# Kernel tuning notes

Measured on AMD Instinct MI355X. Metric: run time of the kernel, lower is better.

The kernel has to match this reference:

```python
import jax, jax.numpy as jnp
import numpy as np

N = 500_000      # total nodes across all graphs in batch
B = 128          # batch_size (number of graphs)
S = 128          # state_size
D = 128          # aggregated_size


def setup_inputs() -> dict:
    key = jax.random.key(0)
    k1, k2, k3, k4, k5, k6 = jax.random.split(key, 6)
    nodes = jax.random.normal(k1, (N, S), dtype=jnp.float32)
    owner_masks = jax.random.randint(k2, (B, N), 0, 2, dtype=jnp.int32)
    # Linear params (torch Linear: y = x @ W.T + b); store W as [in, out] for x @ W
    scale = 1.0 / np.sqrt(S)
    Wt = jax.random.uniform(k3, (S, D), jnp.float32, -scale, scale)
    bt = jax.random.uniform(k4, (D,), jnp.float32, -scale, scale)
    Wg = jax.random.uniform(k5, (S, D), jnp.float32, -scale, scale)
    bg = jax.random.uniform(k6, (D,), jnp.float32, -scale, scale)
    return {"nodes": nodes, "owner_masks": owner_masks,
            "Wt": Wt, "bt": bt, "Wg": Wg, "bg": bg}


def reference(nodes, owner_masks, Wt, bt, Wg, bg):
    # gates = sigmoid(nodes @ Wg + bg)   [N, D]
    gates = jax.nn.sigmoid(nodes @ Wg + bg)
    # data = nodes @ Wt + bt             [N, D]
    data = nodes @ Wt + bt
    # pooled = owner_masks.float() @ (data * gates)   [B, D]
    return owner_masks.astype(jnp.float32) @ (data * gates)
```

## Files before the change

kernel.cpp:

```cpp
#include <hip/hip_runtime.h>


#define NTOT   500000
#define NBLK   512
#define NCHUNK 15625

typedef __attribute__((ext_vector_type(8))) unsigned short ushort8;
typedef __bf16 bf16x8 __attribute__((ext_vector_type(8)));
typedef __attribute__((ext_vector_type(4))) float f32x4;

static __device__ __forceinline__ unsigned short f2bf(float f) {
  unsigned int u = __float_as_uint(f);
  u += 0x7fffu + ((u >> 16) & 1u);
  return (unsigned short)(u >> 16);
}

static __device__ __forceinline__ unsigned long long pack4(unsigned short a, unsigned short b,
                                                           unsigned short c, unsigned short d) {
  return (unsigned long long)a | ((unsigned long long)b << 16) |
         ((unsigned long long)c << 32) | ((unsigned long long)d << 48);
}

template <bool ATOMIC>
__global__ __launch_bounds__(256, 2)
void agg_main(const float* __restrict__ nodes, const int* __restrict__ masks,
              const float* __restrict__ Wt, const float* __restrict__ bt,
              const float* __restrict__ Wg, const float* __restrict__ bg,
              float* __restrict__ outp) {
  __shared__ __align__(16) unsigned short nodes_s[32][136];
  __shared__ __align__(16) unsigned short mask_s[128][40];
  __shared__ __align__(16) unsigned short vt_s[128][40];

  const int tid = threadIdx.x;
  const int lane = tid & 63;
  const int w = tid >> 6;
  const int q = lane >> 4;
  const int r = lane & 15;

  bf16x8 Wf[2][4][2];
  float btr[2], bgr[2];
#pragma unroll
  for (int nt = 0; nt < 2; ++nt) {
    const int d = w * 32 + nt * 16 + r;
    btr[nt] = bt[d];
    bgr[nt] = bg[d];
#pragma unroll
    for (int ks = 0; ks < 4; ++ks) {
      ushort8 ft, fg;
#pragma unroll
      for (int j = 0; j < 8; ++j) {
        const int k = ks * 32 + q * 8 + j;
        ft[j] = f2bf(Wt[k * 128 + d]);
        fg[j] = f2bf(Wg[k * 128 + d]);
      }
      Wf[0][ks][nt] = __builtin_bit_cast(bf16x8, ft);
      Wf[1][ks][nt] = __builtin_bit_cast(bf16x8, fg);
    }
  }

  f32x4 acc[4][4];
  const f32x4 fzero = {0.f, 0.f, 0.f, 0.f};
#pragma unroll
  for (int i = 0; i < 4; ++i)
#pragma unroll
    for (int j = 0; j < 4; ++j) acc[i][j] = fzero;

  const int bid = blockIdx.x;
  const int c0 = (int)(((long long)bid * NCHUNK) / NBLK);
  const int c1 = (int)(((long long)(bid + 1) * NCHUNK) / NBLK);

  float4 nf[4];
  int4 mi[4];
  auto issue = [&](int c) {
    const int k0 = c * 32;
#pragma unroll
    for (int it = 0; it < 4; ++it) {
      const int flat = it * 256 + tid;
      const int nrow = flat >> 5, nc4 = flat & 31;
      nf[it] = *(const float4*)(nodes + (size_t)(k0 + nrow) * 128 + nc4 * 4);
      const int mrow = flat >> 3, mc4 = flat & 7;
      mi[it] = *(const int4*)(masks + (size_t)mrow * NTOT + k0 + mc4 * 4);
    }
  };

  if (c0 < c1) issue(c0);

  for (int c = c0; c < c1; ++c) {
    __syncthreads();
#pragma unroll
    for (int it = 0; it < 4; ++it) {
      const int flat = it * 256 + tid;
      const int nrow = flat >> 5, nc4 = flat & 31;
      *(unsigned long long*)&nodes_s[nrow][nc4 * 4] =
          pack4(f2bf(nf[it].x), f2bf(nf[it].y), f2bf(nf[it].z), f2bf(nf[it].w));
      const int mrow = flat >> 3, mc4 = flat & 7;
      *(unsigned long long*)&mask_s[mrow][mc4 * 4] =
          pack4(f2bf((float)mi[it].x), f2bf((float)mi[it].y),
                f2bf((float)mi[it].z), f2bf((float)mi[it].w));
    }
    __syncthreads();
    if (c + 1 < c1) issue(c + 1);

    f32x4 aD[2][2], aG[2][2];
#pragma unroll
    for (int i = 0; i < 2; ++i)
#pragma unroll
      for (int j = 0; j < 2; ++j) { aD[i][j] = fzero; aG[i][j] = fzero; }
#pragma unroll
    for (int ks = 0; ks < 4; ++ks) {
      bf16x8 a0 = *(const bf16x8*)&nodes_s[r][ks * 32 + q * 8];
      bf16x8 a1 = *(const bf16x8*)&nodes_s[16 + r][ks * 32 + q * 8];
#pragma unroll
      for (int nt = 0; nt < 2; ++nt) {
        aD[0][nt] = __builtin_amdgcn_mfma_f32_16x16x32_bf16(a0, Wf[0][ks][nt], aD[0][nt], 0, 0, 0);
        aD[1][nt] = __builtin_amdgcn_mfma_f32_16x16x32_bf16(a1, Wf[0][ks][nt], aD[1][nt], 0, 0, 0);
        aG[0][nt] = __builtin_amdgcn_mfma_f32_16x16x32_bf16(a0, Wf[1][ks][nt], aG[0][nt], 0, 0, 0);
        aG[1][nt] = __builtin_amdgcn_mfma_f32_16x16x32_bf16(a1, Wf[1][ks][nt], aG[1][nt], 0, 0, 0);
      }
    }

#pragma unroll
    for (int mt = 0; mt < 2; ++mt)
#pragma unroll
      for (int nt = 0; nt < 2; ++nt) {
        const int d = w * 32 + nt * 16 + r;
        unsigned short t[4];
#pragma unroll
        for (int reg = 0; reg < 4; ++reg) {
          const float x = aD[mt][nt][reg] + btr[nt];
          const float g = aG[mt][nt][reg] + bgr[nt];
          t[reg] = f2bf(x / (1.f + __expf(-g)));
        }
        *(unsigned long long*)&vt_s[d][mt * 16 + q * 4] = pack4(t[0], t[1], t[2], t[3]);
      }
    __syncthreads();

    const int mb = (w >> 1) * 64, nb = (w & 1) * 64;
    bf16x8 bfr[4];
#pragma unroll
    for (int nt = 0; nt < 4; ++nt)
      bfr[nt] = *(const bf16x8*)&vt_s[nb + nt * 16 + r][q * 8];
#pragma unroll
    for (int mt = 0; mt < 4; ++mt) {
      bf16x8 af = *(const bf16x8*)&mask_s[mb + mt * 16 + r][q * 8];
#pragma unroll
      for (int nt = 0; nt < 4; ++nt)
        acc[mt][nt] = __builtin_amdgcn_mfma_f32_16x16x32_bf16(af, bfr[nt], acc[mt][nt], 0, 0, 0);
    }
  }

#pragma unroll
  for (int mt = 0; mt < 4; ++mt)
#pragma unroll
    for (int nt = 0; nt < 4; ++nt)
#pragma unroll
      for (int reg = 0; reg < 4; ++reg) {
        const int b = (w >> 1) * 64 + mt * 16 + q * 4 + reg;
        const int d = (w & 1) * 64 + nt * 16 + r;
        if (ATOMIC)
          atomicAdd(&outp[b * 128 + d], acc[mt][nt][reg]);
        else
          outp[(size_t)bid * 16384 + b * 128 + d] = acc[mt][nt][reg];
      }
}

__global__ __launch_bounds__(256)
void agg_reduce(const float* __restrict__ part, float* __restrict__ out) {
  const int gid = blockIdx.x * 256 + threadIdx.x;
  const int i = gid & 16383;
  const int grp = gid >> 14;
  const float* p = part + (size_t)grp * 64 * 16384 + i;
  float s = 0.f;
#pragma unroll 8
  for (int g = 0; g < 64; ++g) s += p[(size_t)g * 16384];
  atomicAdd(&out[i], s);
}

extern "C" void kernel_launch(void* const* d_in, const int* in_sizes, int n_in,
                              void* d_out, int out_size, void* d_ws, size_t ws_size,
                              hipStream_t stream) {
  const float* nodes = (const float*)d_in[0];
  const int*   masks = (const int*)d_in[1];
  const float* Wt    = (const float*)d_in[2];
  const float* bt    = (const float*)d_in[3];
  const float* Wg    = (const float*)d_in[4];
  const float* bg    = (const float*)d_in[5];
  float* out = (float*)d_out;

  hipMemsetAsync(d_out, 0, (size_t)out_size * sizeof(float), stream);

  const size_t need = (size_t)NBLK * 16384 * sizeof(float);
  if (ws_size >= need) {
    agg_main<false><<<NBLK, 256, 0, stream>>>(nodes, masks, Wt, bt, Wg, bg, (float*)d_ws);
    agg_reduce<<<512, 256, 0, stream>>>((const float*)d_ws, out);
  } else {
    agg_main<true><<<NBLK, 256, 0, stream>>>(nodes, masks, Wt, bt, Wg, bg, out);
  }
}
```

Baseline: 523.8 us.

## Feed mask fragments from registers and double-buffer LDS with one barrier per chunk

Masks are now loaded straight into MFMA A-operand registers and turned into bf16 0/1 by bit selection, so the mask LDS tile and its staging pass are gone. The node and value tiles are double-buffered, and the pooling MFMA for chunk i-1 overlaps the projection GEMM for chunk i, cutting barriers from three per chunk to one. The manual float-to-bf16 routine is replaced by native bf16 conversion, and the sigmoid division by a reciprocal. Per-lane mask loads now cover shorter contiguous runs, so global access is less coalesced, and the pipelined register state raises register pressure.

```diff
diff --git a/kernel.cpp b/kernel.cpp
--- a/kernel.cpp
+++ b/kernel.cpp
@@ -7,18 +7,18 @@
 
 typedef __attribute__((ext_vector_type(8))) unsigned short ushort8;
 typedef __bf16 bf16x8 __attribute__((ext_vector_type(8)));
+typedef __bf16 bf16x2 __attribute__((ext_vector_type(2)));
 typedef __attribute__((ext_vector_type(4))) float f32x4;
 
-static __device__ __forceinline__ unsigned short f2bf(float f) {
-  unsigned int u = __float_as_uint(f);
-  u += 0x7fffu + ((u >> 16) & 1u);
-  return (unsigned short)(u >> 16);
-}
-
-static __device__ __forceinline__ unsigned long long pack4(unsigned short a, unsigned short b,
-                                                           unsigned short c, unsigned short d) {
-  return (unsigned long long)a | ((unsigned long long)b << 16) |
-         ((unsigned long long)c << 32) | ((unsigned long long)d << 48);
+static __device__ __forceinline__ unsigned int pkbf(float a, float b) {
+  bf16x2 v;
+  v[0] = (__bf16)a;
+  v[1] = (__bf16)b;
+  return __builtin_bit_cast(unsigned int, v);
+}
+
+static __device__ __forceinline__ unsigned int mkw(int lo, int hi) {
+  return (lo ? 0x3F80u : 0u) | (hi ? 0x3F800000u : 0u);
 }
 
 template <bool ATOMIC>
@@ -27,9 +27,8 @@
               const float* __restrict__ Wt, const float* __restrict__ bt,
               const float* __restrict__ Wg, const float* __restrict__ bg,
               float* __restrict__ outp) {
-  __shared__ __align__(16) unsigned short nodes_s[32][136];
-  __shared__ __align__(16) unsigned short mask_s[128][40];
-  __shared__ __align__(16) unsigned short vt_s[128][40];
+  __shared__ __align__(16) unsigned short nodes_s[2][32][136];
+  __shared__ __align__(16) unsigned short vt_s[2][128][40];
 
   const int tid = threadIdx.x;
   const int lane = tid & 63;
@@ -50,66 +49,88 @@
 #pragma unroll
       for (int j = 0; j < 8; ++j) {
         const int k = ks * 32 + q * 8 + j;
-        ft[j] = f2bf(Wt[k * 128 + d]);
-        fg[j] = f2bf(Wg[k * 128 + d]);
+        ft[j] = __builtin_bit_cast(unsigned short, (__bf16)Wt[k * 128 + d]);
+        fg[j] = __builtin_bit_cast(unsigned short, (__bf16)Wg[k * 128 + d]);
       }
       Wf[0][ks][nt] = __builtin_bit_cast(bf16x8, ft);
       Wf[1][ks][nt] = __builtin_bit_cast(bf16x8, fg);
     }
   }
 
-  f32x4 acc[4][4];
+  f32x4 acc[2][8];
   const f32x4 fzero = {0.f, 0.f, 0.f, 0.f};
 #pragma unroll
-  for (int i = 0; i < 4; ++i)
-#pragma unroll
-    for (int j = 0; j < 4; ++j) acc[i][j] = fzero;
+  for (int i = 0; i < 2; ++i)
+#pragma unroll
+    for (int j = 0; j < 8; ++j) acc[i][j] = fzero;
 
   const int bid = blockIdx.x;
   const int c0 = (int)(((long long)bid * NCHUNK) / NBLK);
   const int c1 = (int)(((long long)(bid + 1) * NCHUNK) / NBLK);
+  const int n = c1 - c0;
+
+  const int* mrow0 = masks + (size_t)(w * 32 + r) * NTOT + q * 8;
+  const int* mrow1 = mrow0 + (size_t)16 * NTOT;
 
   float4 nf[4];
-  int4 mi[4];
-  auto issue = [&](int c) {
+  int4 miA[2][2], miB[2][2];
+
+  auto issue_nodes = [&](int c) {
+    const float4* p = (const float4*)(nodes + (size_t)c * 32 * 128);
+#pragma unroll
+    for (int it = 0; it < 4; ++it) nf[it] = p[it * 256 + tid];
+  };
+
+  auto issue_masks = [&](int4 (&mi)[2][2], int c) {
     const int k0 = c * 32;
+    mi[0][0] = *(const int4*)(mrow0 + k0);
+    mi[0][1] = *(const int4*)(mrow0 + k0 + 4);
+    mi[1][0] = *(const int4*)(mrow1 + k0);
+    mi[1][1] = *(const int4*)(mrow1 + k0 + 4);
+  };
+
+  auto stage = [&](int buf) {
 #pragma unroll
     for (int it = 0; it < 4; ++it) {
       const int flat = it * 256 + tid;
       const int nrow = flat >> 5, nc4 = flat & 31;
-      nf[it] = *(const float4*)(nodes + (size_t)(k0 + nrow) * 128 + nc4 * 4);
-      const int mrow = flat >> 3, mc4 = flat & 7;
-      mi[it] = *(const int4*)(masks + (size_t)mrow * NTOT + k0 + mc4 * 4);
-    }
-  };
-
-  if (c0 < c1) issue(c0);
-
-  for (int c = c0; c < c1; ++c) {
-    __syncthreads();
-#pragma unroll
-    for (int it = 0; it < 4; ++it) {
-      const int flat = it * 256 + tid;
-      const int nrow = flat >> 5, nc4 = flat & 31;
-      *(unsigned long long*)&nodes_s[nrow][nc4 * 4] =
-          pack4(f2bf(nf[it].x), f2bf(nf[it].y), f2bf(nf[it].z), f2bf(nf[it].w));
-      const int mrow = flat >> 3, mc4 = flat & 7;
-      *(unsigned long long*)&mask_s[mrow][mc4 * 4] =
-          pack4(f2bf((float)mi[it].x), f2bf((float)mi[it].y),
-                f2bf((float)mi[it].z), f2bf((float)mi[it].w));
-    }
-    __syncthreads();
-    if (c + 1 < c1) issue(c + 1);
-
+      uint2 u;
+      u.x = pkbf(nf[it].x, nf[it].y);
+      u.y = pkbf(nf[it].z, nf[it].w);
+      *(uint2*)&nodes_s[buf][nrow][nc4 * 4] = u;
+    }
+  };
+
+  auto pool = [&](const int4 (&mi)[2][2], int buf) {
+    uint4 u0, u1;
+    u0.x = mkw(mi[0][0].x, mi[0][0].y);
+    u0.y = mkw(mi[0][0].z, mi[0][0].w);
+    u0.z = mkw(mi[0][1].x, mi[0][1].y);
+    u0.w = mkw(mi[0][1].z, mi[0][1].w);
+    u1.x = mkw(mi[1][0].x, mi[1][0].y);
+    u1.y = mkw(mi[1][0].z, mi[1][0].w);
+    u1.z = mkw(mi[1][1].x, mi[1][1].y);
+    u1.w = mkw(mi[1][1].z, mi[1][1].w);
+    const bf16x8 af0 = __builtin_bit_cast(bf16x8, u0);
+    const bf16x8 af1 = __builtin_bit_cast(bf16x8, u1);
+#pragma unroll
+    for (int nt = 0; nt < 8; ++nt) {
+      const bf16x8 bfr = *(const bf16x8*)&vt_s[buf][nt * 16 + r][q * 8];
+      acc[0][nt] = __builtin_amdgcn_mfma_f32_16x16x32_bf16(af0, bfr, acc[0][nt], 0, 0, 0);
+      acc[1][nt] = __builtin_amdgcn_mfma_f32_16x16x32_bf16(af1, bfr, acc[1][nt], 0, 0, 0);
+    }
+  };
+
+  auto gemm_epi = [&](int buf) {
     f32x4 aD[2][2], aG[2][2];
 #pragma unroll
-    for (int i = 0; i < 2; ++i)
-#pragma unroll
-      for (int j = 0; j < 2; ++j) { aD[i][j] = fzero; aG[i][j] = fzero; }
+    for (int i2 = 0; i2 < 2; ++i2)
+#pragma unroll
+      for (int j2 = 0; j2 < 2; ++j2) { aD[i2][j2] = fzero; aG[i2][j2] = fzero; }
 #pragma unroll
     for (int ks = 0; ks < 4; ++ks) {
-      bf16x8 a0 = *(const bf16x8*)&nodes_s[r][ks * 32 + q * 8];
-      bf16x8 a1 = *(const bf16x8*)&nodes_s[16 + r][ks * 32 + q * 8];
+      const bf16x8 a0 = *(const bf16x8*)&nodes_s[buf][r][ks * 32 + q * 8];
+      const bf16x8 a1 = *(const bf16x8*)&nodes_s[buf][16 + r][ks * 32 + q * 8];
 #pragma unroll
       for (int nt = 0; nt < 2; ++nt) {
         aD[0][nt] = __builtin_amdgcn_mfma_f32_16x16x32_bf16(a0, Wf[0][ks][nt], aD[0][nt], 0, 0, 0);
@@ -118,45 +139,59 @@
         aG[1][nt] = __builtin_amdgcn_mfma_f32_16x16x32_bf16(a1, Wf[1][ks][nt], aG[1][nt], 0, 0, 0);
       }
     }
-
 #pragma unroll
     for (int mt = 0; mt < 2; ++mt)
 #pragma unroll
       for (int nt = 0; nt < 2; ++nt) {
         const int d = w * 32 + nt * 16 + r;
-        unsigned short t[4];
+        float v[4];
 #pragma unroll
         for (int reg = 0; reg < 4; ++reg) {
           const float x = aD[mt][nt][reg] + btr[nt];
           const float g = aG[mt][nt][reg] + bgr[nt];
-          t[reg] = f2bf(x / (1.f + __expf(-g)));
+          v[reg] = x * __builtin_amdgcn_rcpf(1.f + __expf(-g));
         }
-        *(unsigned long long*)&vt_s[d][mt * 16 + q * 4] = pack4(t[0], t[1], t[2], t[3]);
-      }
+        uint2 u;
+        u.x = pkbf(v[0], v[1]);
+        u.y = pkbf(v[2], v[3]);
+        *(uint2*)&vt_s[buf][d][mt * 16 + q * 4] = u;
+      }
+  };
+
+  int i = 0;
+  auto body = [&](int buf, int4 (&mip)[2][2], int4 (&mii)[2][2]) {
+    stage(buf);
     __syncthreads();
-
-    const int mb = (w >> 1) * 64, nb = (w & 1) * 64;
-    bf16x8 bfr[4];
-#pragma unroll
-    for (int nt = 0; nt < 4; ++nt)
-      bfr[nt] = *(const bf16x8*)&vt_s[nb + nt * 16 + r][q * 8];
-#pragma unroll
-    for (int mt = 0; mt < 4; ++mt) {
-      bf16x8 af = *(const bf16x8*)&mask_s[mb + mt * 16 + r][q * 8];
-#pragma unroll
-      for (int nt = 0; nt < 4; ++nt)
-        acc[mt][nt] = __builtin_amdgcn_mfma_f32_16x16x32_bf16(af, bfr[nt], acc[mt][nt], 0, 0, 0);
-    }
-  }
-
-#pragma unroll
-  for (int mt = 0; mt < 4; ++mt)
-#pragma unroll
-    for (int nt = 0; nt < 4; ++nt)
+    const int c = c0 + i;
+    if (i + 1 < n) issue_nodes(c + 1);
+    if (i > 0) pool(mip, buf ^ 1);
+    if (i + 1 < n) issue_masks(mii, c + 1);
+    gemm_epi(buf);
+    ++i;
+  };
+
+  if (n > 0) {
+    issue_nodes(c0);
+    issue_masks(miA, c0);
+  }
+  while (i < n) {
+    body(0, miB, miB);
+    if (i < n) body(1, miA, miA);
+  }
+  __syncthreads();
+  if (n > 0) {
+    if ((n - 1) & 1) pool(miB, 1);
+    else             pool(miA, 0);
+  }
+
+#pragma unroll
+  for (int mt = 0; mt < 2; ++mt)
+#pragma unroll
+    for (int nt = 0; nt < 8; ++nt)
 #pragma unroll
       for (int reg = 0; reg < 4; ++reg) {
-        const int b = (w >> 1) * 64 + mt * 16 + q * 4 + reg;
-        const int d = (w & 1) * 64 + nt * 16 + r;
+        const int b = w * 32 + mt * 16 + q * 4 + reg;
+        const int d = nt * 16 + r;
         if (ATOMIC)
           atomicAdd(&outp[b * 128 + d], acc[mt][nt][reg]);
         else
```

New measurement: 526.6 us. Within noise of the previous version (+0.5%).
